# Kernel tuning notes

Hardware: AMD Instinct MI355X
Metric: run time of the kernel (lower is better)

The kernel has to match this reference:

```python
import jax, jax.numpy as jnp
import numpy as np

N, E = 50000, 800000          # nodes, edges
IN, OUT, ED = 128, 64, 32     # in_dim, out_dim, edge_dim


def setup_inputs() -> dict:
    key = jax.random.key(0)
    ks = jax.random.split(key, 8)
    init = lambda k, shape, fan: jax.random.normal(k, shape, jnp.float32) * np.float32(1.0 / np.sqrt(fan))
    return {
        "x": jax.random.normal(ks[0], (N, IN), jnp.float32),
        "edge_attr": jax.random.normal(ks[1], (E, ED), jnp.float32),
        "edge_index": jax.random.randint(ks[2], (2, E), 0, N),
        "W_fc": init(ks[3], (IN, OUT), IN),
        "b_fc": jnp.zeros((OUT,), jnp.float32),
        "W_attn": init(ks[4], (2 * OUT + ED, 1), 2 * OUT + ED),
        "b_attn": jnp.zeros((1,), jnp.float32),
        "W_edge": init(ks[5], (ED, OUT), ED),
        "b_edge": jnp.zeros((OUT,), jnp.float32),
        "W_self": init(ks[6], (IN, OUT), IN),
        "b_self": jnp.zeros((OUT,), jnp.float32),
    }


def reference(x, edge_attr, edge_index, W_fc, b_fc, W_attn, b_attn,
              W_edge, b_edge, W_self, b_self):
    row, col = edge_index[0], edge_index[1]   # src, dst node ids per edge
    # node transform: z = fc(x)  (batch norm disabled -> identity)
    z = x @ W_fc + b_fc                        # [N, OUT]
    # edge-dependent attention logits: cat(z_src, z_dst, ex) -> scalar
    z2 = jnp.concatenate([z[row], z[col], edge_attr], axis=1)   # [E, 2*OUT+ED]
    e = jax.nn.leaky_relu(z2 @ W_attn + b_attn, negative_slope=0.2)  # [E, 1]
    # edge feature transform for aggregation
    ez = edge_attr @ W_edge + b_edge           # [E, OUT]
    # segment softmax over incoming edges of each destination node
    m = jax.ops.segment_max(e, col, num_segments=N)   # [N, 1]
    m = jnp.where(jnp.isfinite(m), m, 0.0)             # nodes with no in-edges
    p = jnp.exp(e - m[col])                             # [E, 1]
    denom = jax.ops.segment_sum(p, col, num_segments=N)
    alpha = p / jnp.maximum(denom[col], 1e-16)          # [E, 1]
    # attention-weighted aggregation of node messages + edge messages
    h = jax.ops.segment_sum(alpha * (z[row] + ez), col, num_segments=N)  # [N, OUT]
    # self-loop residual with its own transform
    h = h + (x @ W_self + b_self)
    return h
```

## Files before the change

kernel.cpp:

```cpp
#include <hip/hip_runtime.h>

typedef unsigned int uint;
typedef unsigned short u16;
typedef unsigned long long u64;

#define IN_DIM 128
#define OUT_DIM 64
#define ED_DIM 32
#define CAP 64

typedef __bf16 bf16x8 __attribute__((ext_vector_type(8)));
typedef float f32x4 __attribute__((ext_vector_type(4)));

static __device__ __forceinline__ float bf2f(u16 u) {
    return __uint_as_float(((uint)u) << 16);
}
static __device__ __forceinline__ u16 f2bf(float f) {
    uint u = __float_as_uint(f);
    uint r = u + 0x7fffu + ((u >> 16) & 1u);
    return (u16)(r >> 16);
}
static __device__ __forceinline__ float ldf(const void* p, size_t i, bool f32m) {
    return f32m ? ((const float*)p)[i] : bf2f(((const u16*)p)[i]);
}
static __device__ __forceinline__ float rlanef(float v, int l) {
    return __uint_as_float((uint)__builtin_amdgcn_readlane((int)__float_as_uint(v), l));
}
static __device__ __forceinline__ uint rlaneu(uint v, int l) {
    return (uint)__builtin_amdgcn_readlane((int)v, l);
}

__global__ __launch_bounds__(256) void k0_prep(
    const u16* __restrict__ xraw, const void* __restrict__ Wfc,
    const void* __restrict__ Wself, u16* __restrict__ Wt_fc,
    u16* __restrict__ Wt_s, uint* __restrict__ flag)
{
    __shared__ int cnt;
    if (threadIdx.x == 0) cnt = 0;
    __syncthreads();
    float v = bf2f(xraw[threadIdx.x]);
    if (!(fabsf(v) <= 64.f)) atomicAdd(&cnt, 1);
    __syncthreads();
    bool f32m = cnt > 0;
    if (threadIdx.x == 0) flag[0] = f32m ? 1u : 0u;
    for (int i = threadIdx.x; i < IN_DIM * OUT_DIM; i += 256) {
        int j = i & 7, lane = (i >> 3) & 63, frag = i >> 9;
        int kt = frag >> 2, nt = frag & 3;
        int q = lane >> 4, c = lane & 15;
        int k = kt * 32 + q * 8 + j;
        int n = nt * 16 + c;
        int src = k * OUT_DIM + n;
        Wt_fc[i] = f32m ? f2bf(((const float*)Wfc)[src]) : ((const u16*)Wfc)[src];
        Wt_s [i] = f32m ? f2bf(((const float*)Wself)[src]) : ((const u16*)Wself)[src];
    }
}

__global__ __launch_bounds__(256) void k1_mfma(
    const void* __restrict__ x, const u16* __restrict__ Wt_fc,
    const u16* __restrict__ Wt_s, const void* __restrict__ bfc,
    const void* __restrict__ Wattn, const void* __restrict__ bself,
    u16* __restrict__ z_bf, float* __restrict__ hself,
    float* __restrict__ a_src, float* __restrict__ a_dst,
    uint* __restrict__ cursor, const uint* __restrict__ flag, int n_nodes)
{
    bool f32m = flag[0] != 0u;
    int tid = blockIdx.x * 256 + threadIdx.x;
    int stride = gridDim.x * 256;
    for (int i = tid; i < n_nodes; i += stride) cursor[i] = 0u;

    int wave = threadIdx.x >> 6, lane = threadIdx.x & 63;
    int q = lane >> 4, c = lane & 15;
    int nb = blockIdx.x * 64 + wave * 16;
    if (nb >= n_nodes) return;

    f32x4 az[4], as_[4];
    #pragma unroll
    for (int nt = 0; nt < 4; nt++) {
        az[nt]  = (f32x4){0.f, 0.f, 0.f, 0.f};
        as_[nt] = (f32x4){0.f, 0.f, 0.f, 0.f};
    }

    int m = nb + c; if (m >= n_nodes) m = n_nodes - 1;

    #pragma unroll
    for (int kt = 0; kt < 4; kt++) {
        int k0 = kt * 32 + q * 8;
        bf16x8 a;
        if (f32m) {
            const float* xr = (const float*)x + (size_t)m * IN_DIM + k0;
            float4 f0 = *(const float4*)xr;
            float4 f1 = *(const float4*)(xr + 4);
            a[0] = (__bf16)f0.x; a[1] = (__bf16)f0.y; a[2] = (__bf16)f0.z; a[3] = (__bf16)f0.w;
            a[4] = (__bf16)f1.x; a[5] = (__bf16)f1.y; a[6] = (__bf16)f1.z; a[7] = (__bf16)f1.w;
        } else {
            a = *(const bf16x8*)((const u16*)x + (size_t)m * IN_DIM + k0);
        }
        #pragma unroll
        for (int nt = 0; nt < 4; nt++) {
            int fo = ((kt * 4 + nt) * 64 + lane) * 8;
            bf16x8 bf = *(const bf16x8*)(Wt_fc + fo);
            bf16x8 bs = *(const bf16x8*)(Wt_s + fo);
            az[nt]  = __builtin_amdgcn_mfma_f32_16x16x32_bf16(a, bf, az[nt], 0, 0, 0);
            as_[nt] = __builtin_amdgcn_mfma_f32_16x16x32_bf16(a, bs, as_[nt], 0, 0, 0);
        }
    }

    float was[4], wad[4], bz[4], bs[4];
    #pragma unroll
    for (int nt = 0; nt < 4; nt++) {
        was[nt] = ldf(Wattn, nt * 16 + c, f32m);
        wad[nt] = ldf(Wattn, 64 + nt * 16 + c, f32m);
        bz[nt]  = ldf(bfc, nt * 16 + c, f32m);
        bs[nt]  = ldf(bself, nt * 16 + c, f32m);
    }
    #pragma unroll
    for (int reg = 0; reg < 4; reg++) {
        int nn = nb + q * 4 + reg;
        bool ok = nn < n_nodes;
        float ps = 0.f, pd = 0.f;
        #pragma unroll
        for (int nt = 0; nt < 4; nt++) {
            float zv = az[nt][reg] + bz[nt];
            float hv = as_[nt][reg] + bs[nt];
            float zp = __shfl_xor(zv, 1, 64);
            if (ok) {
                hself[(size_t)nn * OUT_DIM + nt * 16 + c] = hv;
                if (!(c & 1)) {
                    uint u = (uint)f2bf(zv) | ((uint)f2bf(zp) << 16);
                    *(uint*)(z_bf + (size_t)nn * OUT_DIM + nt * 16 + c) = u;
                }
            }
            ps = fmaf(zv, was[nt], ps);
            pd = fmaf(zv, wad[nt], pd);
        }
        #pragma unroll
        for (int off = 8; off; off >>= 1) {
            ps += __shfl_xor(ps, off, 64);
            pd += __shfl_xor(pd, off, 64);
        }
        if (ok && c == 0) { a_src[nn] = ps; a_dst[nn] = pd; }
    }
}

__global__ __launch_bounds__(256) void k4_scatter(
    const int* __restrict__ ei, const void* __restrict__ edge_attr,
    const void* __restrict__ Wattn, const void* __restrict__ battn,
    const float* __restrict__ a_src, const float* __restrict__ a_dst,
    uint* __restrict__ cursor, u64* __restrict__ meta,
    u16* __restrict__ ea_bf, const uint* __restrict__ flag,
    int use_ea, int n_edges)
{
    bool f32m = flag[0] != 0u;
    int e = blockIdx.x * 256 + threadIdx.x;
    if (e >= n_edges) return;
    int r = ei[e];
    int c = ei[n_edges + e];
    uint pos = atomicAdd(&cursor[c], 1u);
    float s = a_src[r] + a_dst[c] + ldf(battn, 0, f32m);

    if (f32m) {
        const float* ea = (const float*)edge_attr + (size_t)e * ED_DIM;
        const float* wa = (const float*)Wattn + 128;
        uint wpk[16];
        #pragma unroll
        for (int j = 0; j < 16; j++) {
            float v0 = ea[2 * j], v1 = ea[2 * j + 1];
            s = fmaf(v0, wa[2 * j], fmaf(v1, wa[2 * j + 1], s));
            wpk[j] = (uint)f2bf(v0) | ((uint)f2bf(v1) << 16);
        }
        if (use_ea) {
            uint4* dst = (uint4*)(ea_bf + (size_t)e * ED_DIM);
            dst[0] = make_uint4(wpk[0], wpk[1], wpk[2], wpk[3]);
            dst[1] = make_uint4(wpk[4], wpk[5], wpk[6], wpk[7]);
            dst[2] = make_uint4(wpk[8], wpk[9], wpk[10], wpk[11]);
            dst[3] = make_uint4(wpk[12], wpk[13], wpk[14], wpk[15]);
        }
    } else {
        const uint* ea = (const uint*)((const u16*)edge_attr + (size_t)e * ED_DIM);
        const u16* wa = (const u16*)Wattn + 128;
        #pragma unroll
        for (int j = 0; j < 16; j++) {
            uint u = ea[j];
            s = fmaf(__uint_as_float(u << 16), bf2f(wa[2 * j]),
                fmaf(__uint_as_float(u & 0xffff0000u), bf2f(wa[2 * j + 1]), s));
        }
    }
    float l = s > 0.f ? s : 0.2f * s;
    float p = __expf(l);
    uint pb = (__float_as_uint(p) + 0x40u) >> 7;
    if (pos < CAP)
        meta[((size_t)c << 6) + pos] =
            (u64)(uint)r | ((u64)(uint)e << 18) | ((u64)pb << 39);
}

__global__ __launch_bounds__(256) void k5_agg(
    const void* __restrict__ edge_attr,
    const void* __restrict__ Wedge, const void* __restrict__ bedge,
    const u16* __restrict__ z_bf, const float* __restrict__ hself,
    const uint* __restrict__ cursor, const u64* __restrict__ meta,
    const u16* __restrict__ ea_bf, void* __restrict__ out,
    const uint* __restrict__ flag, int use_ea, int n_nodes)
{
    bool f32m = flag[0] != 0u;
    __shared__ float sWedge[ED_DIM * OUT_DIM];
    for (int i = threadIdx.x; i < ED_DIM * OUT_DIM; i += 256)
        sWedge[i] = ldf(Wedge, i, f32m);
    __syncthreads();

    int lane = threadIdx.x & 63;
    int n = (blockIdx.x * 256 + threadIdx.x) >> 6;
    if (n >= n_nodes) return;

    uint deg = cursor[n];
    if (deg > CAP) deg = CAP;
    float h = hself[(size_t)n * OUT_DIM + lane];

    if (deg > 0) {
        const u64* seg = meta + ((size_t)n << 6);
        bool act = (uint)lane < deg;
        float p_l = 0.f;
        uint eid_l = 0u, row_l = 0u;
        if (act) {
            u64 me = seg[lane];
            row_l = (uint)(me & 0x3FFFFu);
            eid_l = (uint)((me >> 18) & 0x1FFFFFu);
            p_l = __uint_as_float((uint)(me >> 39) << 7);
        }

        float d = p_l;
        #pragma unroll
        for (int off = 32; off; off >>= 1) d += __shfl_xor(d, off, 64);

        int l32 = lane & 31;
        int hi = lane >> 5;
        const float* eaf = (const float*)edge_attr;
        const u16* eab = f32m ? ea_bf : (const u16*)edge_attr;
        bool ea_f32 = f32m && !use_ea;

        float accz = 0.f, accea = 0.f;
        uint pad8 = (deg + 7u) & ~7u;
        for (uint j = 0; j < pad8; j += 8) {
            float pz[8]; uint rz[8], gz[8];
            #pragma unroll
            for (int t = 0; t < 8; t++) {
                pz[t] = rlanef(p_l, (int)(j + t));
                rz[t] = rlaneu(row_l, (int)(j + t));
                gz[t] = rlaneu(eid_l, (int)(j + t));
            }
            float z[8];
            #pragma unroll
            for (int t = 0; t < 8; t++)
                z[t] = bf2f(z_bf[(size_t)rz[t] * OUT_DIM + lane]);
            float va[4], pa[4];
            #pragma unroll
            for (int t = 0; t < 4; t++) {
                uint g = hi ? gz[2 * t + 1] : gz[2 * t];
                pa[t] = hi ? pz[2 * t + 1] : pz[2 * t];
                va[t] = ea_f32 ? eaf[(size_t)g * ED_DIM + l32]
                               : bf2f(eab[(size_t)g * ED_DIM + l32]);
            }
            #pragma unroll
            for (int t = 0; t < 8; t++) accz = fmaf(pz[t], z[t], accz);
            #pragma unroll
            for (int t = 0; t < 4; t++) accea = fmaf(pa[t], va[t], accea);
        }
        accea += __shfl_xor(accea, 32, 64);

        float inv = 1.f / fmaxf(d, 1e-30f);
        float hea = accea * inv;
        float he = ldf(bedge, lane, f32m);
        #pragma unroll
        for (int j = 0; j < ED_DIM; j++) {
            float hj = rlanef(hea, j);
            he = fmaf(hj, sWedge[j * OUT_DIM + lane], he);
        }
        h += accz * inv + he;
    }

    size_t oi = (size_t)n * OUT_DIM + lane;
    if (f32m) ((float*)out)[oi] = h;
    else      ((u16*)out)[oi] = f2bf(h);
}

extern "C" void kernel_launch(void* const* d_in, const int* in_sizes, int n_in,
                              void* d_out, int out_size, void* d_ws, size_t ws_size,
                              hipStream_t stream) {
    const void* x         = d_in[0];
    const void* edge_attr = d_in[1];
    const int*  ei        = (const int*)d_in[2];
    const void* Wfc       = d_in[3];
    const void* bfc       = d_in[4];
    const void* Wattn     = d_in[5];
    const void* battn     = d_in[6];
    const void* Wedge     = d_in[7];
    const void* bedge     = d_in[8];
    const void* Wself     = d_in[9];
    const void* bself     = d_in[10];

    const int N = in_sizes[0] / IN_DIM;
    const int E = in_sizes[1] / ED_DIM;

    char* ws = (char*)d_ws;
    size_t off = 0;
    auto alloc = [&](size_t bytes) -> void* {
        void* p = ws + off;
        off += (bytes + 255) & ~(size_t)255;
        return p;
    };
    u16*   z_bf   = (u16*)  alloc((size_t)N * OUT_DIM * sizeof(u16));
    float* hself  = (float*)alloc((size_t)N * OUT_DIM * sizeof(float));
    float* a_src  = (float*)alloc((size_t)N * sizeof(float));
    float* a_dst  = (float*)alloc((size_t)N * sizeof(float));
    uint*  cursor = (uint*) alloc((size_t)N * sizeof(uint));
    u64*   meta   = (u64*)  alloc((size_t)N * CAP * sizeof(u64));
    u16*   Wt_fc  = (u16*)  alloc((size_t)IN_DIM * OUT_DIM * sizeof(u16));
    u16*   Wt_s   = (u16*)  alloc((size_t)IN_DIM * OUT_DIM * sizeof(u16));
    uint*  flag   = (uint*) alloc(256);

    size_t ea_bytes = (size_t)E * ED_DIM * sizeof(u16);
    int use_ea = (off + ea_bytes + 4096 <= ws_size) ? 1 : 0;
    u16* ea_bf = use_ea ? (u16*)alloc(ea_bytes) : (u16*)ws;

    int mfmaBlocks = (N + 63) / 64;
    int nodeBlocks = (N + 3) / 4;
    int edgeBlocks = (E + 255) / 256;

    k0_prep<<<1, 256, 0, stream>>>((const u16*)x, Wfc, Wself, Wt_fc, Wt_s, flag);
    k1_mfma<<<mfmaBlocks, 256, 0, stream>>>(x, Wt_fc, Wt_s, bfc, Wattn, bself,
                                            z_bf, hself, a_src, a_dst,
                                            cursor, flag, N);
    k4_scatter<<<edgeBlocks, 256, 0, stream>>>(ei, edge_attr, Wattn, battn,
                                               a_src, a_dst, cursor,
                                               meta, ea_bf, flag, use_ea, E);
    k5_agg<<<nodeBlocks, 256, 0, stream>>>(edge_attr, Wedge, bedge,
                                           z_bf, hself, cursor, meta,
                                           ea_bf, d_out, flag, use_ea, N);
}
```

Before: 329.4 us.

## Move edge-attr attention dot product from scatter into aggregation kernel

The scatter kernel no longer reads edge_attr or writes a bf16 copy of it. It stores only the partial logit (a_src+a_dst+bias) in the per-node meta slot, using a nontemporal store. The aggregation kernel now reads edge_attr in fp32 directly, computes the edge_attr·W_attn dot product with a wave shuffle reduction, then applies leaky-relu, exp and the denominator in-loop. This removes one full pass over edge_attr plus the bf16 write and re-read. In exchange, aggregation reads fp32 edge_attr (twice the bytes of the bf16 copy) and adds shuffle reductions per edge pair.

```diff
diff --git a/kernel.cpp b/kernel.cpp
--- a/kernel.cpp
+++ b/kernel.cpp
@@ -143,12 +143,10 @@
 }
 
 __global__ __launch_bounds__(256) void k4_scatter(
-    const int* __restrict__ ei, const void* __restrict__ edge_attr,
-    const void* __restrict__ Wattn, const void* __restrict__ battn,
+    const int* __restrict__ ei, const void* __restrict__ battn,
     const float* __restrict__ a_src, const float* __restrict__ a_dst,
     uint* __restrict__ cursor, u64* __restrict__ meta,
-    u16* __restrict__ ea_bf, const uint* __restrict__ flag,
-    int use_ea, int n_edges)
+    const uint* __restrict__ flag, int n_edges)
 {
     bool f32m = flag[0] != 0u;
     int e = blockIdx.x * 256 + threadIdx.x;
@@ -156,50 +154,20 @@
     int r = ei[e];
     int c = ei[n_edges + e];
     uint pos = atomicAdd(&cursor[c], 1u);
-    float s = a_src[r] + a_dst[c] + ldf(battn, 0, f32m);
-
-    if (f32m) {
-        const float* ea = (const float*)edge_attr + (size_t)e * ED_DIM;
-        const float* wa = (const float*)Wattn + 128;
-        uint wpk[16];
-        #pragma unroll
-        for (int j = 0; j < 16; j++) {
-            float v0 = ea[2 * j], v1 = ea[2 * j + 1];
-            s = fmaf(v0, wa[2 * j], fmaf(v1, wa[2 * j + 1], s));
-            wpk[j] = (uint)f2bf(v0) | ((uint)f2bf(v1) << 16);
-        }
-        if (use_ea) {
-            uint4* dst = (uint4*)(ea_bf + (size_t)e * ED_DIM);
-            dst[0] = make_uint4(wpk[0], wpk[1], wpk[2], wpk[3]);
-            dst[1] = make_uint4(wpk[4], wpk[5], wpk[6], wpk[7]);
-            dst[2] = make_uint4(wpk[8], wpk[9], wpk[10], wpk[11]);
-            dst[3] = make_uint4(wpk[12], wpk[13], wpk[14], wpk[15]);
-        }
-    } else {
-        const uint* ea = (const uint*)((const u16*)edge_attr + (size_t)e * ED_DIM);
-        const u16* wa = (const u16*)Wattn + 128;
-        #pragma unroll
-        for (int j = 0; j < 16; j++) {
-            uint u = ea[j];
-            s = fmaf(__uint_as_float(u << 16), bf2f(wa[2 * j]),
-                fmaf(__uint_as_float(u & 0xffff0000u), bf2f(wa[2 * j + 1]), s));
-        }
-    }
-    float l = s > 0.f ? s : 0.2f * s;
-    float p = __expf(l);
-    uint pb = (__float_as_uint(p) + 0x40u) >> 7;
-    if (pos < CAP)
-        meta[((size_t)c << 6) + pos] =
-            (u64)(uint)r | ((u64)(uint)e << 18) | ((u64)pb << 39);
+    float s0 = a_src[r] + a_dst[c] + ldf(battn, 0, f32m);
+    uint sb = (__float_as_uint(s0) + 0x40u) >> 7;
+    if (pos < CAP) {
+        u64 slot = (u64)(uint)r | ((u64)(uint)e << 18) | ((u64)sb << 39);
+        __builtin_nontemporal_store(slot, &meta[((size_t)c << 6) + pos]);
+    }
 }
 
 __global__ __launch_bounds__(256) void k5_agg(
-    const void* __restrict__ edge_attr,
+    const void* __restrict__ edge_attr, const void* __restrict__ Wattn,
     const void* __restrict__ Wedge, const void* __restrict__ bedge,
     const u16* __restrict__ z_bf, const float* __restrict__ hself,
     const uint* __restrict__ cursor, const u64* __restrict__ meta,
-    const u16* __restrict__ ea_bf, void* __restrict__ out,
-    const uint* __restrict__ flag, int use_ea, int n_nodes)
+    void* __restrict__ out, const uint* __restrict__ flag, int n_nodes)
 {
     bool f32m = flag[0] != 0u;
     __shared__ float sWedge[ED_DIM * OUT_DIM];
@@ -208,8 +176,12 @@
     __syncthreads();
 
     int lane = threadIdx.x & 63;
+    int l32 = lane & 31;
+    int hi = lane >> 5;
     int n = (blockIdx.x * 256 + threadIdx.x) >> 6;
     if (n >= n_nodes) return;
+
+    float wa = ldf(Wattn, 2 * OUT_DIM + l32, f32m);
 
     uint deg = cursor[n];
     if (deg > CAP) deg = CAP;
@@ -218,51 +190,62 @@
     if (deg > 0) {
         const u64* seg = meta + ((size_t)n << 6);
         bool act = (uint)lane < deg;
-        float p_l = 0.f;
+        float s0_l = 0.f;
         uint eid_l = 0u, row_l = 0u;
         if (act) {
             u64 me = seg[lane];
             row_l = (uint)(me & 0x3FFFFu);
             eid_l = (uint)((me >> 18) & 0x1FFFFFu);
-            p_l = __uint_as_float((uint)(me >> 39) << 7);
-        }
-
-        float d = p_l;
-        #pragma unroll
-        for (int off = 32; off; off >>= 1) d += __shfl_xor(d, off, 64);
-
-        int l32 = lane & 31;
-        int hi = lane >> 5;
+            s0_l  = __uint_as_float((uint)(me >> 39) << 7);
+        }
+
         const float* eaf = (const float*)edge_attr;
-        const u16* eab = f32m ? ea_bf : (const u16*)edge_attr;
-        bool ea_f32 = f32m && !use_ea;
-
-        float accz = 0.f, accea = 0.f;
+        const u16*  eab = (const u16*)edge_attr;
+
+        float d = 0.f, accz = 0.f, accea = 0.f;
         uint pad8 = (deg + 7u) & ~7u;
         for (uint j = 0; j < pad8; j += 8) {
-            float pz[8]; uint rz[8], gz[8];
+            float sz[8]; uint rz[8], gz[8];
             #pragma unroll
             for (int t = 0; t < 8; t++) {
-                pz[t] = rlanef(p_l, (int)(j + t));
+                sz[t] = rlanef(s0_l, (int)(j + t));
                 rz[t] = rlaneu(row_l, (int)(j + t));
                 gz[t] = rlaneu(eid_l, (int)(j + t));
             }
+            float va[4];
+            #pragma unroll
+            for (int t = 0; t < 4; t++) {
+                uint g = hi ? gz[2 * t + 1] : gz[2 * t];
+                va[t] = f32m ? eaf[(size_t)g * ED_DIM + l32]
+                             : bf2f(eab[(size_t)g * ED_DIM + l32]);
+            }
             float z[8];
             #pragma unroll
             for (int t = 0; t < 8; t++)
                 z[t] = bf2f(z_bf[(size_t)rz[t] * OUT_DIM + lane]);
-            float va[4], pa[4];
+            float pz[8];
             #pragma unroll
             for (int t = 0; t < 4; t++) {
-                uint g = hi ? gz[2 * t + 1] : gz[2 * t];
-                pa[t] = hi ? pz[2 * t + 1] : pz[2 * t];
-                va[t] = ea_f32 ? eaf[(size_t)g * ED_DIM + l32]
-                               : bf2f(eab[(size_t)g * ED_DIM + l32]);
-            }
-            #pragma unroll
-            for (int t = 0; t < 8; t++) accz = fmaf(pz[t], z[t], accz);
-            #pragma unroll
-            for (int t = 0; t < 4; t++) accea = fmaf(pa[t], va[t], accea);
+                float dt = va[t] * wa;
+                dt += __shfl_xor(dt, 1, 64);
+                dt += __shfl_xor(dt, 2, 64);
+                dt += __shfl_xor(dt, 4, 64);
+                dt += __shfl_xor(dt, 8, 64);
+                dt += __shfl_xor(dt, 16, 64);
+                float s = dt + (hi ? sz[2 * t + 1] : sz[2 * t]);
+                float l = s > 0.f ? s : 0.2f * s;
+                float p = __expf(l);
+                uint eidx = j + 2u * t + (uint)hi;
+                p = (eidx < deg) ? p : 0.f;
+                accea = fmaf(p, va[t], accea);
+                pz[2 * t]     = rlanef(p, 0);
+                pz[2 * t + 1] = rlanef(p, 32);
+            }
+            #pragma unroll
+            for (int t = 0; t < 8; t++) {
+                d += pz[t];
+                accz = fmaf(pz[t], z[t], accz);
+            }
         }
         accea += __shfl_xor(accea, 32, 64);
 
@@ -317,10 +300,6 @@
     u16*   Wt_s   = (u16*)  alloc((size_t)IN_DIM * OUT_DIM * sizeof(u16));
     uint*  flag   = (uint*) alloc(256);
 
-    size_t ea_bytes = (size_t)E * ED_DIM * sizeof(u16);
-    int use_ea = (off + ea_bytes + 4096 <= ws_size) ? 1 : 0;
-    u16* ea_bf = use_ea ? (u16*)alloc(ea_bytes) : (u16*)ws;
-
     int mfmaBlocks = (N + 63) / 64;
     int nodeBlocks = (N + 3) / 4;
     int edgeBlocks = (E + 255) / 256;
@@ -329,10 +308,9 @@
     k1_mfma<<<mfmaBlocks, 256, 0, stream>>>(x, Wt_fc, Wt_s, bfc, Wattn, bself,
                                             z_bf, hself, a_src, a_dst,
                                             cursor, flag, N);
-    k4_scatter<<<edgeBlocks, 256, 0, stream>>>(ei, edge_attr, Wattn, battn,
-                                               a_src, a_dst, cursor,
-                                               meta, ea_bf, flag, use_ea, E);
-    k5_agg<<<nodeBlocks, 256, 0, stream>>>(edge_attr, Wedge, bedge,
+    k4_scatter<<<edgeBlocks, 256, 0, stream>>>(ei, battn, a_src, a_dst,
+                                               cursor, meta, flag, E);
+    k5_agg<<<nodeBlocks, 256, 0, stream>>>(edge_attr, Wattn, Wedge, bedge,
                                            z_bf, hself, cursor, meta,
-                                           ea_bf, d_out, flag, use_ea, N);
-}
+                                           d_out, flag, N);
+}
```

Result: slower. 395.2 us (+19.9%).

## Move edge-attr attention dot and bf16 packing into node GEMM kernel

Applied to the files above, without the earlier changes.

Moves the per-edge edge_attr·W_attn dot product and the bf16 repacking of edge_attr out of the scatter kernel and into the node-transform MFMA kernel. Each thread there handles edges in a grid-stride loop after its node tile, so the edge streaming can overlap the GEMM work. The partial logit goes to a new per-edge float buffer that the scatter kernel reads. This shortens the atomic-heavy scatter kernel, at the cost of an extra E-float write and read and a heavier k1.

```diff
diff --git a/kernel.cpp b/kernel.cpp
--- a/kernel.cpp
+++ b/kernel.cpp
@@ -11,6 +11,7 @@
 
 typedef __bf16 bf16x8 __attribute__((ext_vector_type(8)));
 typedef float f32x4 __attribute__((ext_vector_type(4)));
+typedef uint uint4v __attribute__((ext_vector_type(4)));
 
 static __device__ __forceinline__ float bf2f(u16 u) {
     return __uint_as_float(((uint)u) << 16);
@@ -59,9 +60,12 @@
     const void* __restrict__ x, const u16* __restrict__ Wt_fc,
     const u16* __restrict__ Wt_s, const void* __restrict__ bfc,
     const void* __restrict__ Wattn, const void* __restrict__ bself,
+    const void* __restrict__ edge_attr, float* __restrict__ pp,
+    u16* __restrict__ ea_bf,
     u16* __restrict__ z_bf, float* __restrict__ hself,
     float* __restrict__ a_src, float* __restrict__ a_dst,
-    uint* __restrict__ cursor, const uint* __restrict__ flag, int n_nodes)
+    uint* __restrict__ cursor, const uint* __restrict__ flag,
+    int use_ea, int n_nodes, int n_edges)
 {
     bool f32m = flag[0] != 0u;
     int tid = blockIdx.x * 256 + threadIdx.x;
@@ -71,84 +75,122 @@
     int wave = threadIdx.x >> 6, lane = threadIdx.x & 63;
     int q = lane >> 4, c = lane & 15;
     int nb = blockIdx.x * 64 + wave * 16;
-    if (nb >= n_nodes) return;
-
-    f32x4 az[4], as_[4];
-    #pragma unroll
-    for (int nt = 0; nt < 4; nt++) {
-        az[nt]  = (f32x4){0.f, 0.f, 0.f, 0.f};
-        as_[nt] = (f32x4){0.f, 0.f, 0.f, 0.f};
+
+    if (nb < n_nodes) {
+        f32x4 az[4], as_[4];
+        #pragma unroll
+        for (int nt = 0; nt < 4; nt++) {
+            az[nt]  = (f32x4){0.f, 0.f, 0.f, 0.f};
+            as_[nt] = (f32x4){0.f, 0.f, 0.f, 0.f};
+        }
+
+        int m = nb + c; if (m >= n_nodes) m = n_nodes - 1;
+
+        #pragma unroll
+        for (int kt = 0; kt < 4; kt++) {
+            int k0 = kt * 32 + q * 8;
+            bf16x8 a;
+            if (f32m) {
+                const float* xr = (const float*)x + (size_t)m * IN_DIM + k0;
+                float4 f0 = *(const float4*)xr;
+                float4 f1 = *(const float4*)(xr + 4);
+                a[0] = (__bf16)f0.x; a[1] = (__bf16)f0.y; a[2] = (__bf16)f0.z; a[3] = (__bf16)f0.w;
+                a[4] = (__bf16)f1.x; a[5] = (__bf16)f1.y; a[6] = (__bf16)f1.z; a[7] = (__bf16)f1.w;
+            } else {
+                a = *(const bf16x8*)((const u16*)x + (size_t)m * IN_DIM + k0);
+            }
+            #pragma unroll
+            for (int nt = 0; nt < 4; nt++) {
+                int fo = ((kt * 4 + nt) * 64 + lane) * 8;
+                bf16x8 bf = *(const bf16x8*)(Wt_fc + fo);
+                bf16x8 bs = *(const bf16x8*)(Wt_s + fo);
+                az[nt]  = __builtin_amdgcn_mfma_f32_16x16x32_bf16(a, bf, az[nt], 0, 0, 0);
+                as_[nt] = __builtin_amdgcn_mfma_f32_16x16x32_bf16(a, bs, as_[nt], 0, 0, 0);
+            }
+        }
+
+        float was[4], wad[4], bz[4], bs[4];
+        #pragma unroll
+        for (int nt = 0; nt < 4; nt++) {
+            was[nt] = ldf(Wattn, nt * 16 + c, f32m);
+            wad[nt] = ldf(Wattn, 64 + nt * 16 + c, f32m);
+            bz[nt]  = ldf(bfc, nt * 16 + c, f32m);
+            bs[nt]  = ldf(bself, nt * 16 + c, f32m);
+        }
+        #pragma unroll
+        for (int reg = 0; reg < 4; reg++) {
+            int nn = nb + q * 4 + reg;
+            bool ok = nn < n_nodes;
+            float ps = 0.f, pd = 0.f;
+            #pragma unroll
+            for (int nt = 0; nt < 4; nt++) {
+                float zv = az[nt][reg] + bz[nt];
+                float hv = as_[nt][reg] + bs[nt];
+                float zp = __shfl_xor(zv, 1, 64);
+                if (ok) {
+                    hself[(size_t)nn * OUT_DIM + nt * 16 + c] = hv;
+                    if (!(c & 1)) {
+                        uint u = (uint)f2bf(zv) | ((uint)f2bf(zp) << 16);
+                        *(uint*)(z_bf + (size_t)nn * OUT_DIM + nt * 16 + c) = u;
+                    }
+                }
+                ps = fmaf(zv, was[nt], ps);
+                pd = fmaf(zv, wad[nt], pd);
+            }
+            #pragma unroll
+            for (int off = 8; off; off >>= 1) {
+                ps += __shfl_xor(ps, off, 64);
+                pd += __shfl_xor(pd, off, 64);
+            }
+            if (ok && c == 0) { a_src[nn] = ps; a_dst[nn] = pd; }
+        }
     }
 
-    int m = nb + c; if (m >= n_nodes) m = n_nodes - 1;
-
-    #pragma unroll
-    for (int kt = 0; kt < 4; kt++) {
-        int k0 = kt * 32 + q * 8;
-        bf16x8 a;
-        if (f32m) {
-            const float* xr = (const float*)x + (size_t)m * IN_DIM + k0;
-            float4 f0 = *(const float4*)xr;
-            float4 f1 = *(const float4*)(xr + 4);
-            a[0] = (__bf16)f0.x; a[1] = (__bf16)f0.y; a[2] = (__bf16)f0.z; a[3] = (__bf16)f0.w;
-            a[4] = (__bf16)f1.x; a[5] = (__bf16)f1.y; a[6] = (__bf16)f1.z; a[7] = (__bf16)f1.w;
-        } else {
-            a = *(const bf16x8*)((const u16*)x + (size_t)m * IN_DIM + k0);
-        }
-        #pragma unroll
-        for (int nt = 0; nt < 4; nt++) {
-            int fo = ((kt * 4 + nt) * 64 + lane) * 8;
-            bf16x8 bf = *(const bf16x8*)(Wt_fc + fo);
-            bf16x8 bs = *(const bf16x8*)(Wt_s + fo);
-            az[nt]  = __builtin_amdgcn_mfma_f32_16x16x32_bf16(a, bf, az[nt], 0, 0, 0);
-            as_[nt] = __builtin_amdgcn_mfma_f32_16x16x32_bf16(a, bs, as_[nt], 0, 0, 0);
+    if (f32m) {
+        const float* wa = (const float*)Wattn + 2 * OUT_DIM;
+        for (int e = tid; e < n_edges; e += stride) {
+            const float* ea = (const float*)edge_attr + (size_t)e * ED_DIM;
+            float s = 0.f;
+            uint wpk[16];
+            #pragma unroll
+            for (int j = 0; j < 16; j++) {
+                float v0 = ea[2 * j], v1 = ea[2 * j + 1];
+                s = fmaf(v0, wa[2 * j], fmaf(v1, wa[2 * j + 1], s));
+                wpk[j] = (uint)f2bf(v0) | ((uint)f2bf(v1) << 16);
+            }
+            pp[e] = s;
+            if (use_ea) {
+                uint4v* dst = (uint4v*)(ea_bf + (size_t)e * ED_DIM);
+                #pragma unroll
+                for (int qq = 0; qq < 4; qq++) {
+                    uint4v w = {wpk[4 * qq], wpk[4 * qq + 1],
+                                wpk[4 * qq + 2], wpk[4 * qq + 3]};
+                    dst[qq] = w;
+                }
+            }
+        }
+    } else {
+        const u16* wa = (const u16*)Wattn + 2 * OUT_DIM;
+        for (int e = tid; e < n_edges; e += stride) {
+            const uint* ea = (const uint*)((const u16*)edge_attr + (size_t)e * ED_DIM);
+            float s = 0.f;
+            #pragma unroll
+            for (int j = 0; j < 16; j++) {
+                uint u = ea[j];
+                s = fmaf(__uint_as_float(u << 16), bf2f(wa[2 * j]),
+                    fmaf(__uint_as_float(u & 0xffff0000u), bf2f(wa[2 * j + 1]), s));
+            }
+            pp[e] = s;
         }
     }
-
-    float was[4], wad[4], bz[4], bs[4];
-    #pragma unroll
-    for (int nt = 0; nt < 4; nt++) {
-        was[nt] = ldf(Wattn, nt * 16 + c, f32m);
-        wad[nt] = ldf(Wattn, 64 + nt * 16 + c, f32m);
-        bz[nt]  = ldf(bfc, nt * 16 + c, f32m);
-        bs[nt]  = ldf(bself, nt * 16 + c, f32m);
-    }
-    #pragma unroll
-    for (int reg = 0; reg < 4; reg++) {
-        int nn = nb + q * 4 + reg;
-        bool ok = nn < n_nodes;
-        float ps = 0.f, pd = 0.f;
-        #pragma unroll
-        for (int nt = 0; nt < 4; nt++) {
-            float zv = az[nt][reg] + bz[nt];
-            float hv = as_[nt][reg] + bs[nt];
-            float zp = __shfl_xor(zv, 1, 64);
-            if (ok) {
-                hself[(size_t)nn * OUT_DIM + nt * 16 + c] = hv;
-                if (!(c & 1)) {
-                    uint u = (uint)f2bf(zv) | ((uint)f2bf(zp) << 16);
-                    *(uint*)(z_bf + (size_t)nn * OUT_DIM + nt * 16 + c) = u;
-                }
-            }
-            ps = fmaf(zv, was[nt], ps);
-            pd = fmaf(zv, wad[nt], pd);
-        }
-        #pragma unroll
-        for (int off = 8; off; off >>= 1) {
-            ps += __shfl_xor(ps, off, 64);
-            pd += __shfl_xor(pd, off, 64);
-        }
-        if (ok && c == 0) { a_src[nn] = ps; a_dst[nn] = pd; }
-    }
 }
 
 __global__ __launch_bounds__(256) void k4_scatter(
-    const int* __restrict__ ei, const void* __restrict__ edge_attr,
-    const void* __restrict__ Wattn, const void* __restrict__ battn,
+    const int* __restrict__ ei, const float* __restrict__ pp,
+    const void* __restrict__ battn,
     const float* __restrict__ a_src, const float* __restrict__ a_dst,
     uint* __restrict__ cursor, u64* __restrict__ meta,
-    u16* __restrict__ ea_bf, const uint* __restrict__ flag,
-    int use_ea, int n_edges)
+    const uint* __restrict__ flag, int n_edges)
 {
     bool f32m = flag[0] != 0u;
     int e = blockIdx.x * 256 + threadIdx.x;
@@ -156,35 +198,7 @@
     int r = ei[e];
     int c = ei[n_edges + e];
     uint pos = atomicAdd(&cursor[c], 1u);
-    float s = a_src[r] + a_dst[c] + ldf(battn, 0, f32m);
-
-    if (f32m) {
-        const float* ea = (const float*)edge_attr + (size_t)e * ED_DIM;
-        const float* wa = (const float*)Wattn + 128;
-        uint wpk[16];
-        #pragma unroll
-        for (int j = 0; j < 16; j++) {
-            float v0 = ea[2 * j], v1 = ea[2 * j + 1];
-            s = fmaf(v0, wa[2 * j], fmaf(v1, wa[2 * j + 1], s));
-            wpk[j] = (uint)f2bf(v0) | ((uint)f2bf(v1) << 16);
-        }
-        if (use_ea) {
-            uint4* dst = (uint4*)(ea_bf + (size_t)e * ED_DIM);
-            dst[0] = make_uint4(wpk[0], wpk[1], wpk[2], wpk[3]);
-            dst[1] = make_uint4(wpk[4], wpk[5], wpk[6], wpk[7]);
-            dst[2] = make_uint4(wpk[8], wpk[9], wpk[10], wpk[11]);
-            dst[3] = make_uint4(wpk[12], wpk[13], wpk[14], wpk[15]);
-        }
-    } else {
-        const uint* ea = (const uint*)((const u16*)edge_attr + (size_t)e * ED_DIM);
-        const u16* wa = (const u16*)Wattn + 128;
-        #pragma unroll
-        for (int j = 0; j < 16; j++) {
-            uint u = ea[j];
-            s = fmaf(__uint_as_float(u << 16), bf2f(wa[2 * j]),
-                fmaf(__uint_as_float(u & 0xffff0000u), bf2f(wa[2 * j + 1]), s));
-        }
-    }
+    float s = a_src[r] + a_dst[c] + pp[e] + ldf(battn, 0, f32m);
     float l = s > 0.f ? s : 0.2f * s;
     float p = __expf(l);
     uint pb = (__float_as_uint(p) + 0x40u) >> 7;
@@ -313,6 +327,7 @@
     float* a_dst  = (float*)alloc((size_t)N * sizeof(float));
     uint*  cursor = (uint*) alloc((size_t)N * sizeof(uint));
     u64*   meta   = (u64*)  alloc((size_t)N * CAP * sizeof(u64));
+    float* pp     = (float*)alloc((size_t)E * sizeof(float));
     u16*   Wt_fc  = (u16*)  alloc((size_t)IN_DIM * OUT_DIM * sizeof(u16));
     u16*   Wt_s   = (u16*)  alloc((size_t)IN_DIM * OUT_DIM * sizeof(u16));
     uint*  flag   = (uint*) alloc(256);
@@ -327,11 +342,11 @@
 
     k0_prep<<<1, 256, 0, stream>>>((const u16*)x, Wfc, Wself, Wt_fc, Wt_s, flag);
     k1_mfma<<<mfmaBlocks, 256, 0, stream>>>(x, Wt_fc, Wt_s, bfc, Wattn, bself,
+                                            edge_attr, pp, ea_bf,
                                             z_bf, hself, a_src, a_dst,
-                                            cursor, flag, N);
-    k4_scatter<<<edgeBlocks, 256, 0, stream>>>(ei, edge_attr, Wattn, battn,
-                                               a_src, a_dst, cursor,
-                                               meta, ea_bf, flag, use_ea, E);
+                                            cursor, flag, use_ea, N, E);
+    k4_scatter<<<edgeBlocks, 256, 0, stream>>>(ei, pp, battn, a_src, a_dst,
+                                               cursor, meta, flag, E);
     k5_agg<<<nodeBlocks, 256, 0, stream>>>(edge_attr, Wedge, bedge,
                                            z_bf, hself, cursor, meta,
                                            ea_bf, d_out, flag, use_ea, N);
```

After: 352.7 us. 7.1% more time.
